# Kernel optimization log

Hardware: AMD Instinct MI355X
Metric: run time of the kernel (lower is better)

## Reference

```python
import jax, jax.numpy as jnp
import numpy as np

B, N, M = 16, 4096, 4096

def setup_inputs() -> dict:
    key = jax.random.key(0)
    k1, k2, k3 = jax.random.split(key, 3)
    src_points = jax.random.normal(k1, (B, N, 3), dtype=jnp.float32)
    tgt_points = jax.random.normal(k2, (B, M, 3), dtype=jnp.float32)
    weights = jax.random.uniform(k3, (B,), dtype=jnp.float32)
    return {"src_points": src_points, "tgt_points": tgt_points, "weights": weights}

def reference(src_points, tgt_points, weights):
    # Pairwise squared distances per batch: [B, N, M]
    # ||s - t||^2 = ||s||^2 + ||t||^2 - 2 s.t  (single dense intermediate)
    s2 = jnp.sum(src_points * src_points, axis=-1)  # [B, N]
    t2 = jnp.sum(tgt_points * tgt_points, axis=-1)  # [B, M]
    cross = jnp.einsum('bnd,bmd->bnm', src_points, tgt_points)  # [B, N, M]
    d2 = s2[:, :, None] + t2[:, None, :] - 2.0 * cross          # [B, N, M]
    d2 = jnp.maximum(d2, 0.0)  # numerical guard
    # Bidirectional chamfer: mean of nearest-neighbor squared distances
    d_src_to_tgt = jnp.mean(jnp.min(d2, axis=2), axis=1)  # [B]
    d_tgt_to_src = jnp.mean(jnp.min(d2, axis=1), axis=1)  # [B]
    distances = d_src_to_tgt + d_tgt_to_src               # [B]
    distances = distances * weights
    return jnp.mean(distances)  # reduction='mean'
```

## Files before the change

kernel.cpp:

```cpp
#include <hip/hip_runtime.h>

#define BQ 16
#define NP 4096
#define MP 4096

constexpr int TPB = 256;
constexpr int WAVES = 4;
constexpr int FR = 2;
constexpr int COLS_PER_BLOCK = 32 * FR * WAVES;
constexpr int ROWSPLIT = 4;
constexpr int GROUPS_PER_BLOCK = (MP / 32) / ROWSPLIT;

typedef __bf16 bf16x8 __attribute__((ext_vector_type(8)));
typedef float f32x16 __attribute__((ext_vector_type(16)));

union Frag {
    unsigned short u[8];
    bf16x8 v;
    int4 i4;
};

__device__ inline unsigned short f2bf(float f) {
    unsigned u = __float_as_uint(f);
    return (unsigned short)((u + 0x7FFFu + ((u >> 16) & 1u)) >> 16);
}
__device__ inline float bf2f(unsigned short h) {
    return __uint_as_float(((unsigned)h) << 16);
}

__device__ inline float mintree16(const f32x16& d) {
    float m0 = fminf(fminf(d[0], d[1]), d[2]);
    float m1 = fminf(fminf(d[3], d[4]), d[5]);
    float m2 = fminf(fminf(d[6], d[7]), d[8]);
    float m3 = fminf(fminf(d[9], d[10]), d[11]);
    float m4 = fminf(fminf(d[12], d[13]), d[14]);
    return fminf(fminf(fminf(m0, m1), m2), fminf(fminf(m3, m4), d[15]));
}

__global__ __launch_bounds__(TPB) void chamfer_prep_kernel(
    const float* __restrict__ srcp, const float* __restrict__ tgtp,
    unsigned short* __restrict__ atab, unsigned short* __restrict__ btab,
    unsigned int* __restrict__ minbuf, float* __restrict__ out) {
    const int idx = blockIdx.x * TPB + threadIdx.x;
    const int gy  = idx >> 12;
    const int t   = idx & 4095;
    const int dir = gy >> 4, b = gy & 15;
    const unsigned short ONE = 0x3F80;

    {
        const float* rows = dir ? (srcp + (size_t)b * NP * 3)
                                : (tgtp + (size_t)b * MP * 3);
        const float* p = rows + (size_t)t * 3;
        float x = p[0], y = p[1], z = p[2];
        unsigned short xh = f2bf(x), yh = f2bf(y), zh = f2bf(z);
        unsigned short xl = f2bf(x - bf2f(xh));
        unsigned short yl = f2bf(y - bf2f(yh));
        unsigned short zl = f2bf(z - bf2f(zh));
        float t2 = fmaf(x, x, fmaf(y, y, z * z));
        unsigned short t2h = f2bf(t2), t2l = f2bf(t2 - bf2f(t2h));
        Frag p0, p1;
        p0.u[0] = xh; p0.u[1] = yh; p0.u[2] = zh;
        p0.u[3] = xh; p0.u[4] = yh; p0.u[5] = zh;
        p0.u[6] = xl; p0.u[7] = yl;
        p1.u[0] = zl; p1.u[1] = t2h; p1.u[2] = t2l;
        p1.u[3] = ONE; p1.u[4] = ONE; p1.u[5] = 0; p1.u[6] = 0; p1.u[7] = 0;
        unsigned short* dst =
            atab + ((size_t)gy << 16) + ((t >> 5) << 9) + ((t & 31) << 4);
        *(int4*)(dst)     = p0.i4;
        *(int4*)(dst + 8) = p1.i4;
    }

    {
        const float* cols = dir ? (tgtp + (size_t)b * MP * 3)
                                : (srcp + (size_t)b * NP * 3);
        const float* p = cols + (size_t)t * 3;
        float x = p[0], y = p[1], z = p[2];
        unsigned short uh0 = f2bf(-2.0f * x), uh1 = f2bf(-2.0f * y), uh2 = f2bf(-2.0f * z);
        unsigned short ul0 = f2bf(-2.0f * x - bf2f(uh0));
        unsigned short ul1 = f2bf(-2.0f * y - bf2f(uh1));
        unsigned short ul2 = f2bf(-2.0f * z - bf2f(uh2));
        float s2 = fmaf(x, x, fmaf(y, y, z * z));
        unsigned short s2h = f2bf(s2), s2l = f2bf(s2 - bf2f(s2h));
        Frag q0, q1;
        q0.u[0] = uh0; q0.u[1] = uh1; q0.u[2] = uh2;
        q0.u[3] = ul0; q0.u[4] = ul1; q0.u[5] = ul2;
        q0.u[6] = uh0; q0.u[7] = uh1;
        q1.u[0] = uh2; q1.u[1] = ONE; q1.u[2] = ONE;
        q1.u[3] = s2h; q1.u[4] = s2l; q1.u[5] = 0; q1.u[6] = 0; q1.u[7] = 0;
        unsigned short* dst = btab + ((size_t)gy << 16) + ((size_t)t << 4);
        *(int4*)(dst)     = q0.i4;
        *(int4*)(dst + 8) = q1.i4;
    }

    minbuf[idx] = 0x7F800000u;
    if (idx == 0) out[0] = 0.0f;
}

__global__ __launch_bounds__(TPB) void chamfer_main_kernel(
    const unsigned short* __restrict__ atab,
    const unsigned short* __restrict__ btab,
    unsigned int* __restrict__ minbuf) {
    const int gy = blockIdx.z;
    unsigned int* mb = minbuf + ((size_t)gy << 12);

    const int tid  = threadIdx.x;
    const int lane = tid & 63;
    const int half = lane >> 5;
    const int col  = lane & 31;
    const int wave = tid >> 6;

    const int c0 = blockIdx.x * COLS_PER_BLOCK + wave * (FR * 32) + col;
    Frag b0, b1;
    b0.i4 = *(const int4*)(btab + ((size_t)gy << 16) + ((size_t)c0 << 4) + (half << 3));
    b1.i4 = *(const int4*)(btab + ((size_t)gy << 16) + ((size_t)(c0 + 32) << 4) + (half << 3));

    float acc0 = __int_as_float(0x7F800000);
    float acc1 = __int_as_float(0x7F800000);

    const f32x16 zc = {};

    const unsigned short* lptr = atab + ((size_t)gy << 16) +
                                 ((size_t)blockIdx.y * GROUPS_PER_BLOCK << 9) +
                                 (col << 4) + (half << 3);

    Frag a;
    a.i4 = *(const int4*)(lptr);

    for (int g = 0; g < GROUPS_PER_BLOCK; ++g) {
        f32x16 d0 = __builtin_amdgcn_mfma_f32_32x32x16_bf16(a.v, b0.v, zc, 0, 0, 0);
        f32x16 d1 = __builtin_amdgcn_mfma_f32_32x32x16_bf16(a.v, b1.v, zc, 0, 0, 0);
        if (g + 1 < GROUPS_PER_BLOCK)
            a.i4 = *(const int4*)(lptr + ((size_t)(g + 1) << 9));
        acc0 = fminf(acc0, mintree16(d0));
        acc1 = fminf(acc1, mintree16(d1));
    }

    {
        float m = fminf(acc0, __shfl_xor(acc0, 32, 64));
        m = fmaxf(m, 0.0f);
        if (lane < 32) atomicMin(&mb[c0], __float_as_uint(m));
    }
    {
        float m = fminf(acc1, __shfl_xor(acc1, 32, 64));
        m = fmaxf(m, 0.0f);
        if (lane < 32) atomicMin(&mb[c0 + 32], __float_as_uint(m));
    }
}

__global__ __launch_bounds__(TPB) void chamfer_reduce_kernel(
    const float* __restrict__ minbuf, const float* __restrict__ weights,
    float* __restrict__ out) {
    const int idx = blockIdx.x;
    const int b = idx & 15;
    const float* m0 = minbuf + ((size_t)idx << 12);

    float s = 0.0f;
    for (int i = threadIdx.x; i < 4096; i += TPB) s += m0[i];
#pragma unroll
    for (int off = 32; off > 0; off >>= 1) s += __shfl_down(s, off, 64);

    __shared__ float red[TPB / 64];
    if ((threadIdx.x & 63) == 0) red[threadIdx.x >> 6] = s;
    __syncthreads();
    if (threadIdx.x == 0) {
        float tot = red[0] + red[1] + red[2] + red[3];
        atomicAdd(out, weights[b] * tot * (1.0f / (4096.0f * (float)BQ)));
    }
}

__global__ void chamfer_zero_kernel(float* __restrict__ out) { out[0] = 0.0f; }

__global__ __launch_bounds__(TPB) void chamfer_fb_kernel(
    const float* __restrict__ srcp, const float* __restrict__ tgtp,
    const float* __restrict__ wts, float* __restrict__ out) {
    const int gy = blockIdx.y, dir = gy >> 4, b = gy & 15;
    const float* S = dir ? (tgtp + (size_t)b * MP * 3) : (srcp + (size_t)b * NP * 3);
    const float* T = dir ? (srcp + (size_t)b * NP * 3) : (tgtp + (size_t)b * MP * 3);
    const int tid = threadIdx.x, lane = tid & 63, half = lane >> 5,
              col = lane & 31, wave = tid >> 6;
    __shared__ unsigned short sh[256 * 16];
    __shared__ float partial[WAVES];
    const unsigned short ONE = 0x3F80;
    Frag bfr[2];
#pragma unroll
    for (int f = 0; f < 2; ++f) {
        const int sidx = blockIdx.x * 256 + (wave * 2 + f) * 32 + col;
        const float* sp = S + (size_t)sidx * 3;
        float x = sp[0], y = sp[1], z = sp[2];
        unsigned short uh0 = f2bf(-2.0f * x), uh1 = f2bf(-2.0f * y), uh2 = f2bf(-2.0f * z);
        unsigned short ul0 = f2bf(-2.0f * x - bf2f(uh0));
        unsigned short ul1 = f2bf(-2.0f * y - bf2f(uh1));
        unsigned short ul2 = f2bf(-2.0f * z - bf2f(uh2));
        float s2 = fmaf(x, x, fmaf(y, y, z * z));
        unsigned short s2h = f2bf(s2), s2l = f2bf(s2 - bf2f(s2h));
        if (half == 0) {
            bfr[f].u[0] = uh0; bfr[f].u[1] = uh1; bfr[f].u[2] = uh2;
            bfr[f].u[3] = ul0; bfr[f].u[4] = ul1; bfr[f].u[5] = ul2;
            bfr[f].u[6] = uh0; bfr[f].u[7] = uh1;
        } else {
            bfr[f].u[0] = uh2; bfr[f].u[1] = ONE; bfr[f].u[2] = ONE;
            bfr[f].u[3] = s2h; bfr[f].u[4] = s2l;
            bfr[f].u[5] = 0;   bfr[f].u[6] = 0;  bfr[f].u[7] = 0;
        }
    }
    float accm[2] = {__int_as_float(0x7F800000), __int_as_float(0x7F800000)};
    const f32x16 zc = {};
    const int sub = tid >> 5, row = tid & 31;
    float cx, cy, cz;
    { const float* tp = T + (size_t)tid * 3; cx = tp[0]; cy = tp[1]; cz = tp[2]; }
    for (int c = 0; c < MP / 256; ++c) {
        {
            unsigned short xh = f2bf(cx), yh = f2bf(cy), zh = f2bf(cz);
            unsigned short xl = f2bf(cx - bf2f(xh));
            unsigned short yl = f2bf(cy - bf2f(yh));
            unsigned short zl = f2bf(cz - bf2f(zh));
            float t2 = fmaf(cx, cx, fmaf(cy, cy, cz * cz));
            unsigned short t2h = f2bf(t2), t2l = f2bf(t2 - bf2f(t2h));
            Frag p0, p1;
            p0.u[0] = xh; p0.u[1] = yh; p0.u[2] = zh;
            p0.u[3] = xh; p0.u[4] = yh; p0.u[5] = zh;
            p0.u[6] = xl; p0.u[7] = yl;
            p1.u[0] = zl; p1.u[1] = t2h; p1.u[2] = t2l;
            p1.u[3] = ONE; p1.u[4] = ONE; p1.u[5] = 0; p1.u[6] = 0; p1.u[7] = 0;
            *(int4*)&sh[((sub * 2 + 0) * 32 + row) * 8] = p0.i4;
            *(int4*)&sh[((sub * 2 + 1) * 32 + row) * 8] = p1.i4;
        }
        __syncthreads();
        if (c + 1 < MP / 256) {
            const float* tp = T + (size_t)((c + 1) * 256 + tid) * 3;
            cx = tp[0]; cy = tp[1]; cz = tp[2];
        }
#pragma unroll
        for (int sc = 0; sc < 8; ++sc) {
            Frag a;
            a.i4 = *(const int4*)&sh[((sc * 2 + half) * 32 + col) * 8];
#pragma unroll
            for (int f = 0; f < 2; ++f) {
                f32x16 d = __builtin_amdgcn_mfma_f32_32x32x16_bf16(a.v, bfr[f].v, zc, 0, 0, 0);
                accm[f] = fminf(accm[f], mintree16(d));
            }
        }
        __syncthreads();
    }
    float tot = 0.0f;
#pragma unroll
    for (int f = 0; f < 2; ++f) {
        float m = fminf(accm[f], __shfl_xor(accm[f], 32, 64));
        tot += fmaxf(m, 0.0f);
    }
#pragma unroll
    for (int off = 32; off > 0; off >>= 1) tot += __shfl_xor(tot, off, 64);
    if (lane == 0) partial[wave] = tot * 0.5f;
    __syncthreads();
    if (tid == 0) {
        float v = partial[0] + partial[1] + partial[2] + partial[3];
        atomicAdd(out, v * wts[b] * (1.0f / ((float)NP * (float)BQ)));
    }
}

extern "C" void kernel_launch(void* const* d_in, const int* in_sizes, int n_in,
                              void* d_out, int out_size, void* d_ws, size_t ws_size,
                              hipStream_t stream) {
    const float* src = (const float*)d_in[0];
    const float* tgt = (const float*)d_in[1];
    const float* wts = (const float*)d_in[2];
    float* out = (float*)d_out;

    const size_t MINBUF_BYTES = (size_t)2 * BQ * 4096 * 4;
    const size_t TABLE_BYTES  = (size_t)2 * BQ * 4096 * 32;

    if (ws_size >= MINBUF_BYTES + 2 * TABLE_BYTES) {
        unsigned int* minbuf = (unsigned int*)d_ws;
        unsigned short* atab = (unsigned short*)((char*)d_ws + MINBUF_BYTES);
        unsigned short* btab = (unsigned short*)((char*)d_ws + MINBUF_BYTES + TABLE_BYTES);

        chamfer_prep_kernel<<<(2 * BQ * 4096) / TPB, TPB, 0, stream>>>(
            src, tgt, atab, btab, minbuf, out);

        dim3 grid(NP / COLS_PER_BLOCK, ROWSPLIT, 2 * BQ);
        chamfer_main_kernel<<<grid, TPB, 0, stream>>>(atab, btab, minbuf);

        chamfer_reduce_kernel<<<2 * BQ, TPB, 0, stream>>>(
            (const float*)minbuf, wts, out);
    } else {
        chamfer_zero_kernel<<<1, 1, 0, stream>>>(out);
        dim3 grid(NP / 256, 2 * BQ);
        chamfer_fb_kernel<<<grid, TPB, 0, stream>>>(src, tgt, wts, out);
    }
}
```

Measured before the change: 92.89 us.

## Stage A-fragment rows through double-buffered LDS with async global-to-LDS loads

The main kernel now copies each block's A-table rows into shared memory in 8 KB chunks using global_load_lds DMA, double-buffered with a barrier per chunk. The MFMA loop then reads its A fragments from LDS instead of issuing a per-wave global load each iteration. This is meant to hide global memory latency and stop the four waves from loading the same rows separately. In exchange it adds __syncthreads per chunk and 16 KB of LDS per block, which may reduce occupancy. The shared array in the fallback kernel is renamed.

```diff
diff --git a/kernel.cpp b/kernel.cpp
--- a/kernel.cpp
+++ b/kernel.cpp
@@ -9,7 +9,9 @@
 constexpr int FR = 2;
 constexpr int COLS_PER_BLOCK = 32 * FR * WAVES;
 constexpr int ROWSPLIT = 4;
-constexpr int GROUPS_PER_BLOCK = (MP / 32) / ROWSPLIT;
+constexpr int ROWS_PER_BLOCK = MP / ROWSPLIT;
+constexpr int CHUNK_ROWS = 256;
+constexpr int NCHUNK = ROWS_PER_BLOCK / CHUNK_ROWS;
 
 typedef __bf16 bf16x8 __attribute__((ext_vector_type(8)));
 typedef float f32x16 __attribute__((ext_vector_type(16)));
@@ -35,6 +37,12 @@
     float m3 = fminf(fminf(d[9], d[10]), d[11]);
     float m4 = fminf(fminf(d[12], d[13]), d[14]);
     return fminf(fminf(fminf(m0, m1), m2), fminf(fminf(m3, m4), d[15]));
+}
+
+__device__ inline void dma16(const void* g, void* l) {
+    __builtin_amdgcn_global_load_lds(
+        (const __attribute__((address_space(1))) unsigned int*)g,
+        (__attribute__((address_space(3))) unsigned int*)l, 16, 0, 0);
 }
 
 __global__ __launch_bounds__(TPB) void chamfer_prep_kernel(
@@ -109,6 +117,8 @@
     const int col  = lane & 31;
     const int wave = tid >> 6;
 
+    __shared__ char sh[2 * 8192];
+
     const int c0 = blockIdx.x * COLS_PER_BLOCK + wave * (FR * 32) + col;
     Frag b0, b1;
     b0.i4 = *(const int4*)(btab + ((size_t)gy << 16) + ((size_t)c0 << 4) + (half << 3));
@@ -116,23 +126,38 @@
 
     float acc0 = __int_as_float(0x7F800000);
     float acc1 = __int_as_float(0x7F800000);
-
     const f32x16 zc = {};
 
-    const unsigned short* lptr = atab + ((size_t)gy << 16) +
-                                 ((size_t)blockIdx.y * GROUPS_PER_BLOCK << 9) +
-                                 (col << 4) + (half << 3);
-
-    Frag a;
-    a.i4 = *(const int4*)(lptr);
-
-    for (int g = 0; g < GROUPS_PER_BLOCK; ++g) {
-        f32x16 d0 = __builtin_amdgcn_mfma_f32_32x32x16_bf16(a.v, b0.v, zc, 0, 0, 0);
-        f32x16 d1 = __builtin_amdgcn_mfma_f32_32x32x16_bf16(a.v, b1.v, zc, 0, 0, 0);
-        if (g + 1 < GROUPS_PER_BLOCK)
-            a.i4 = *(const int4*)(lptr + ((size_t)(g + 1) << 9));
-        acc0 = fminf(acc0, mintree16(d0));
-        acc1 = fminf(acc1, mintree16(d1));
+    const char* ga = (const char*)atab + ((size_t)gy << 17) +
+                     ((size_t)blockIdx.y << 15);
+
+    {
+        const char* g = ga;
+        char* l = sh + wave * 1024;
+        dma16(g + tid * 16, l);
+        dma16(g + tid * 16 + 4096, l + 4096);
+    }
+
+    for (int c = 0; c < NCHUNK; ++c) {
+        __syncthreads();
+
+        if (c + 1 < NCHUNK) {
+            const char* g = ga + (size_t)(c + 1) * 8192;
+            char* l = sh + ((c + 1) & 1) * 8192 + wave * 1024;
+            dma16(g + tid * 16, l);
+            dma16(g + tid * 16 + 4096, l + 4096);
+        }
+
+        const char* buf = sh + (c & 1) * 8192 + col * 32 + half * 16;
+#pragma unroll
+        for (int g = 0; g < CHUNK_ROWS / 32; ++g) {
+            Frag a;
+            a.i4 = *(const int4*)(buf + g * 1024);
+            f32x16 d0 = __builtin_amdgcn_mfma_f32_32x32x16_bf16(a.v, b0.v, zc, 0, 0, 0);
+            f32x16 d1 = __builtin_amdgcn_mfma_f32_32x32x16_bf16(a.v, b1.v, zc, 0, 0, 0);
+            acc0 = fminf(acc0, mintree16(d0));
+            acc1 = fminf(acc1, mintree16(d1));
+        }
     }
 
     {
@@ -178,7 +203,7 @@
     const float* T = dir ? (srcp + (size_t)b * NP * 3) : (tgtp + (size_t)b * MP * 3);
     const int tid = threadIdx.x, lane = tid & 63, half = lane >> 5,
               col = lane & 31, wave = tid >> 6;
-    __shared__ unsigned short sh[256 * 16];
+    __shared__ unsigned short shl[256 * 16];
     __shared__ float partial[WAVES];
     const unsigned short ONE = 0x3F80;
     Frag bfr[2];
@@ -222,8 +247,8 @@
             p0.u[6] = xl; p0.u[7] = yl;
             p1.u[0] = zl; p1.u[1] = t2h; p1.u[2] = t2l;
             p1.u[3] = ONE; p1.u[4] = ONE; p1.u[5] = 0; p1.u[6] = 0; p1.u[7] = 0;
-            *(int4*)&sh[((sub * 2 + 0) * 32 + row) * 8] = p0.i4;
-            *(int4*)&sh[((sub * 2 + 1) * 32 + row) * 8] = p1.i4;
+            *(int4*)&shl[((sub * 2 + 0) * 32 + row) * 8] = p0.i4;
+            *(int4*)&shl[((sub * 2 + 1) * 32 + row) * 8] = p1.i4;
         }
         __syncthreads();
         if (c + 1 < MP / 256) {
@@ -233,7 +258,7 @@
 #pragma unroll
         for (int sc = 0; sc < 8; ++sc) {
             Frag a;
-            a.i4 = *(const int4*)&sh[((sc * 2 + half) * 32 + col) * 8];
+            a.i4 = *(const int4*)&shl[((sc * 2 + half) * 32 + col) * 8];
 #pragma unroll
             for (int f = 0; f < 2; ++f) {
                 f32x16 d = __builtin_amdgcn_mfma_f32_32x32x16_bf16(a.v, bfr[f].v, zc, 0, 0, 0);
```

After: 122.4 us. +31.8%, slower.
